# Kernel tuning notes

Measured on AMD Instinct MI355X. Metric: run time of the kernel, lower is better.

## Reference

```python
import jax, jax.numpy as jnp
import numpy as np

B, S, HID = 1, 2048, 4096
NH, NKV, HD = 32, 8, 128
N_REP = NH // NKV
EPS = 1e-5
ROPE_THETA = 500000.0


def setup_inputs() -> dict:
    key = jax.random.key(0)
    ks = jax.random.split(key, 16)
    s = 0.02
    return {
        "hidden_states": jax.random.normal(ks[0], (B, S, HID), jnp.float32),
        "Wq": jax.random.normal(ks[1], (NH * HD, HID), jnp.float32) * s,
        "bq": jnp.zeros((NH * HD,), jnp.float32),
        "Wk": jax.random.normal(ks[2], (NKV * HD, HID), jnp.float32) * s,
        "bk": jnp.zeros((NKV * HD,), jnp.float32),
        "Wv": jax.random.normal(ks[3], (NKV * HD, HID), jnp.float32) * s,
        "bv": jnp.zeros((NKV * HD,), jnp.float32),
        "Wo": jax.random.normal(ks[4], (HID, HID), jnp.float32) * s,
        "bo": jnp.zeros((HID,), jnp.float32),
        "qn_g": jnp.ones((HD,), jnp.float32),
        "qn_b": jnp.zeros((HD,), jnp.float32),
        "kn_g": jnp.ones((HD,), jnp.float32),
        "kn_b": jnp.zeros((HD,), jnp.float32),
    }


def _layernorm(x, g, b):
    mu = jnp.mean(x, axis=-1, keepdims=True)
    var = jnp.var(x, axis=-1, keepdims=True)
    return (x - mu) * jax.lax.rsqrt(var + EPS) * g + b


def _rope_tables(seq_len, dtype):
    inv_freq = 1.0 / ROPE_THETA ** (jnp.arange(0, HD, 2, dtype=jnp.float32) / HD)
    pos = jnp.arange(seq_len, dtype=jnp.float32)
    freqs = pos[:, None] * inv_freq[None, :]          # (S, HD/2)
    emb = jnp.concatenate([freqs, freqs], axis=-1)    # (S, HD)
    return jnp.cos(emb).astype(dtype), jnp.sin(emb).astype(dtype)


def _rotate_half(x):
    x1, x2 = x[..., : HD // 2], x[..., HD // 2 :]
    return jnp.concatenate([-x2, x1], axis=-1)


def reference(hidden_states, Wq, bq, Wk, bk, Wv, bv, Wo, bo, qn_g, qn_b, kn_g, kn_b):
    x = hidden_states
    q = (x @ Wq.T + bq).reshape(B, S, NH, HD)
    k = (x @ Wk.T + bk).reshape(B, S, NKV, HD)
    v = (x @ Wv.T + bv).reshape(B, S, NKV, HD)
    # QK-Norm (LayerNorm over head_dim)
    q = _layernorm(q, qn_g, qn_b).transpose(0, 2, 1, 3)  # (B, NH, S, HD)
    k = _layernorm(k, kn_g, kn_b).transpose(0, 2, 1, 3)  # (B, NKV, S, HD)
    v = v.transpose(0, 2, 1, 3)
    # RoPE
    cos, sin = _rope_tables(S, x.dtype)  # (S, HD) each, broadcast over B, heads
    q = q * cos + _rotate_half(q) * sin
    k = k * cos + _rotate_half(k) * sin
    # GQA: repeat KV heads
    k = jnp.repeat(k, N_REP, axis=1)  # (B, NH, S, HD)
    v = jnp.repeat(v, N_REP, axis=1)
    # Causal attention
    scores = jnp.einsum("bhqd,bhkd->bhqk", q, k) / jnp.sqrt(jnp.float32(HD)).astype(x.dtype)
    causal = jnp.tril(jnp.ones((S, S), bool))
    scores = jnp.where(causal, scores, jnp.finfo(scores.dtype).min)
    attn = jax.nn.softmax(scores, axis=-1)
    out = jnp.einsum("bhqk,bhkd->bhqd", attn, v)
    out = out.transpose(0, 2, 1, 3).reshape(B, S, HID)
    return out @ Wo.T + bo
```

## Files before the change

kernel.cpp:

```cpp
#include <hip/hip_runtime.h>

typedef __bf16 bf16;
typedef __bf16 bf16x8 __attribute__((ext_vector_type(8)));
typedef __bf16 bf16x4 __attribute__((ext_vector_type(4)));
typedef float f32x4 __attribute__((ext_vector_type(4)));

#define S_LEN 2048
#define HID 4096
#define NH 32
#define NKV 8
#define HD 128
#define QSTR 6144
#define SCALE 0.08838834764831845f
#define QSCL 0.1275164918918885f
#define M2C 16.33f

template <int V> struct IC { static constexpr int value = V; };

__device__ __forceinline__ bf16x8 load8(const bf16* p) { return *(const bf16x8*)p; }
__device__ __forceinline__ bf16x8 load8(const float* p) {
    float4 a = *(const float4*)p;
    float4 b = *(const float4*)(p + 4);
    bf16x8 r;
    r[0] = (bf16)a.x; r[1] = (bf16)a.y; r[2] = (bf16)a.z; r[3] = (bf16)a.w;
    r[4] = (bf16)b.x; r[5] = (bf16)b.y; r[6] = (bf16)b.z; r[7] = (bf16)b.w;
    return r;
}

__device__ __forceinline__ void load_lds16(const bf16* g, bf16* l) {
    __builtin_amdgcn_global_load_lds(
        (const __attribute__((address_space(1))) void*)g,
        (__attribute__((address_space(3))) void*)l, 16, 0, 0);
}

template <int C> __device__ __forceinline__ void vmwait_if() {
    if constexpr (C >= 0) asm volatile("s_waitcnt vmcnt(%0)" ::"n"(C) : "memory");
}

__device__ __forceinline__ void lgkm0() {
    asm volatile("s_waitcnt lgkmcnt(0)" ::: "memory");
    __builtin_amdgcn_sched_barrier(0);
}

__global__ __launch_bounds__(256) void cvt5(const float* __restrict__ x,
                                            const float* __restrict__ Wq,
                                            const float* __restrict__ Wk,
                                            const float* __restrict__ Wv,
                                            const float* __restrict__ Wo,
                                            bf16* __restrict__ xb,
                                            bf16* __restrict__ Wqkv,
                                            bf16* __restrict__ Wob) {
    int i = blockIdx.x * 256 + threadIdx.x;
    const float* src;
    bf16* dst;
    if (i < 1048576)      { src = x  + (size_t)i * 8;              dst = xb + (size_t)i * 8; }
    else if (i < 3145728) { size_t j = i - 1048576; src = Wq + j * 8; dst = Wqkv + j * 8; }
    else if (i < 3670016) { size_t j = i - 3145728; src = Wk + j * 8; dst = Wqkv + 16777216 + j * 8; }
    else if (i < 4194304) { size_t j = i - 3670016; src = Wv + j * 8; dst = Wqkv + 20971520 + j * 8; }
    else                  { size_t j = i - 4194304; src = Wo + j * 8; dst = Wob + j * 8; }
    *(bf16x8*)dst = load8(src);
}

template <int BMODE, typename TO>
__global__ __launch_bounds__(512, 2) void gemmQ(const bf16* __restrict__ A,
                                                const bf16* __restrict__ Bw,
                                                const float* __restrict__ b0,
                                                const float* __restrict__ b1,
                                                const float* __restrict__ b2,
                                                TO* __restrict__ out,
                                                int N, int K) {
    __shared__ __align__(16) bf16 AS[4 * 128 * 64];
    __shared__ __align__(16) bf16 BS[4 * 128 * 64];

    const int tid  = threadIdx.x;
    const int wave = tid >> 6;
    const int lane = tid & 63;
    const int quad = lane >> 4;
    const int l16  = lane & 15;
    const int wm   = wave >> 2;
    const int wn   = wave & 3;

    const int gx   = gridDim.x;
    const int nwg  = gx * gridDim.y;
    const int orig = blockIdx.y * gx + blockIdx.x;
    int wg = orig;
    if ((nwg & 7) == 0) wg = (orig & 7) * (nwg >> 3) + (orig >> 3);
    const int row0 = (wg / gx) * 256;
    const int col0 = (wg % gx) * 256;

    auto stageA = [&](int h, int bufv, int kt) {
#pragma unroll
        for (int j = 0; j < 2; ++j) {
            int c = j * 512 + tid;
            int r = c >> 3, pg = c & 7;
            int g = pg ^ (r & 7);
            int gr = (r >> 6) * 128 + h * 64 + (r & 63);
            load_lds16(&A[(size_t)(row0 + gr) * K + kt * 64 + g * 8],
                       &AS[(bufv * 2 + h) * 8192 + c * 8]);
        }
    };
    auto stageB = [&](int nh, int bufv, int kt) {
#pragma unroll
        for (int j = 0; j < 2; ++j) {
            int c = j * 512 + tid;
            int r = c >> 3, pg = c & 7;
            int g = pg ^ (r & 7);
            int gc = (r >> 5) * 64 + nh * 32 + (r & 31);
            load_lds16(&Bw[(size_t)(col0 + gc) * K + kt * 64 + g * 8],
                       &BS[(bufv * 2 + nh) * 8192 + c * 8]);
        }
    };

    f32x4 acc[8][4];
#pragma unroll
    for (int a = 0; a < 8; ++a)
#pragma unroll
        for (int b = 0; b < 4; ++b) { f32x4 z = {0.f, 0.f, 0.f, 0.f}; acc[a][b] = z; }

    bf16x8 afr[4][2];
    bf16x8 bfr[2][2][2];

    auto loadAh = [&](int h, int bufv) {
#pragma unroll
        for (int mi = 0; mi < 4; ++mi)
#pragma unroll
            for (int ks = 0; ks < 2; ++ks) {
                int r = wm * 64 + mi * 16 + l16;
                int gg = ks * 4 + quad;
                afr[mi][ks] = *(const bf16x8*)&AS[(bufv * 2 + h) * 8192 + r * 64 +
                                                  ((gg ^ (r & 7)) << 3)];
            }
    };
    auto loadBh = [&](auto cNQ, int bufv) {
        constexpr int NQ = decltype(cNQ)::value;
#pragma unroll
        for (int ni = 0; ni < 2; ++ni)
#pragma unroll
            for (int ks = 0; ks < 2; ++ks) {
                int r = wn * 32 + ni * 16 + l16;
                int gg = ks * 4 + quad;
                bfr[NQ][ni][ks] = *(const bf16x8*)&BS[(bufv * 2 + NQ) * 8192 + r * 64 +
                                                      ((gg ^ (r & 7)) << 3)];
            }
    };
    auto mmac = [&](auto cMQ, auto cNQ) {
        constexpr int MQ = decltype(cMQ)::value, NQ = decltype(cNQ)::value;
        __builtin_amdgcn_s_setprio(1);
#pragma unroll
        for (int mi = 0; mi < 4; ++mi)
#pragma unroll
            for (int ni = 0; ni < 2; ++ni)
#pragma unroll
                for (int ks = 0; ks < 2; ++ks)
                    acc[MQ * 4 + mi][NQ * 2 + ni] = __builtin_amdgcn_mfma_f32_16x16x32_bf16(
                        afr[mi][ks], bfr[NQ][ni][ks], acc[MQ * 4 + mi][NQ * 2 + ni], 0, 0, 0);
        __builtin_amdgcn_s_setprio(0);
    };

    auto run_iter = [&](int t0, auto cST, auto cV3, auto cV7) {
        constexpr bool ST = decltype(cST)::value != 0;
        stageA(1, 1, t0 + 1);
        loadAh(0, 0);
        loadBh(IC<0>{}, 0);
        __builtin_amdgcn_s_barrier();
        lgkm0();
        mmac(IC<0>{}, IC<0>{});
        __builtin_amdgcn_s_barrier();
        if constexpr (ST) stageA(0, 0, t0 + 2);
        loadBh(IC<1>{}, 0);
        __builtin_amdgcn_s_barrier();
        lgkm0();
        mmac(IC<0>{}, IC<1>{});
        __builtin_amdgcn_s_barrier();
        if constexpr (ST) stageB(0, 0, t0 + 2);
        loadAh(1, 0);
        __builtin_amdgcn_s_barrier();
        lgkm0();
        mmac(IC<1>{}, IC<0>{});
        __builtin_amdgcn_s_barrier();
        if constexpr (ST) stageB(1, 0, t0 + 2);
        __builtin_amdgcn_s_barrier();
        mmac(IC<1>{}, IC<1>{});
        vmwait_if<decltype(cV3)::value>();
        __builtin_amdgcn_s_barrier();
        if constexpr (ST) stageA(1, 0, t0 + 2);
        loadAh(0, 1);
        loadBh(IC<0>{}, 1);
        __builtin_amdgcn_s_barrier();
        lgkm0();
        mmac(IC<0>{}, IC<0>{});
        __builtin_amdgcn_s_barrier();
        if constexpr (ST) stageA(0, 1, t0 + 3);
        loadBh(IC<1>{}, 1);
        __builtin_amdgcn_s_barrier();
        lgkm0();
        mmac(IC<0>{}, IC<1>{});
        __builtin_amdgcn_s_barrier();
        if constexpr (ST) stageB(0, 1, t0 + 3);
        loadAh(1, 1);
        __builtin_amdgcn_s_barrier();
        lgkm0();
        mmac(IC<1>{}, IC<0>{});
        __builtin_amdgcn_s_barrier();
        if constexpr (ST) stageB(1, 1, t0 + 3);
        __builtin_amdgcn_s_barrier();
        mmac(IC<1>{}, IC<1>{});
        vmwait_if<decltype(cV7)::value>();
        __builtin_amdgcn_s_barrier();
    };

    stageA(0, 0, 0); stageB(0, 0, 0); stageB(1, 0, 0); stageA(1, 0, 0);
    stageA(0, 1, 1); stageB(0, 1, 1); stageB(1, 1, 1);
    vmwait_if<6>();
    __builtin_amdgcn_s_barrier();

    const int NT = K >> 6;
    for (int t0 = 0; t0 < NT - 2; t0 += 2)
        run_iter(t0, IC<1>{}, IC<6>{}, IC<6>{});
    run_iter(NT - 2, IC<0>{}, IC<0>{}, IC<-1>{});

#pragma unroll
    for (int mq = 0; mq < 2; ++mq)
#pragma unroll
        for (int nq = 0; nq < 2; ++nq)
#pragma unroll
            for (int ni = 0; ni < 2; ++ni) {
                int n = col0 + wn * 64 + nq * 32 + ni * 16 + l16;
                float bv;
                if (BMODE == 0) bv = b0[n];
                else bv = (n < 4096) ? b0[n] : ((n < 5120) ? b1[n - 4096] : b2[n - 5120]);
#pragma unroll
                for (int mi = 0; mi < 4; ++mi) {
                    int m = row0 + wm * 128 + mq * 64 + mi * 16 + quad * 4;
#pragma unroll
                    for (int reg = 0; reg < 4; ++reg)
                        out[(size_t)(m + reg) * N + n] =
                            (TO)(acc[mq * 4 + mi][nq * 2 + ni][reg] + bv);
                }
            }
}

template <int BM, int BN, int WM, int WN, int BMODE, typename TO>
__global__ __launch_bounds__(512, 2) void gemm8(const bf16* __restrict__ A,
                                                const bf16* __restrict__ Bw,
                                                const float* __restrict__ b0,
                                                const float* __restrict__ b1,
                                                const float* __restrict__ b2,
                                                TO* __restrict__ out,
                                                int N, int K) {
    constexpr int RW  = BM / WM;
    constexpr int CW  = BN / WN;
    constexpr int FM  = RW / 16;
    constexpr int FN  = CW / 16;
    constexpr int FMH = FM / 2;
    constexpr int FNH0 = (FN + 1) / 2, FNH1 = FN - FNH0;
    constexpr int SZ0 = FNH0 * 16, SZ1 = FNH1 * 16;
    constexpr int AROWS_H = BM / 2;
    constexpr int B0ROWS = WN * SZ0, B1ROWS = WN * SZ1;
    constexpr int LA  = AROWS_H / 64;
    constexpr int LB0 = B0ROWS / 64, LB1 = B1ROWS / 64;
    constexpr int V0  = 2 * LA + LB0;
    constexpr int V3  = 2 * LA + LB0 + LB1;
    constexpr int V3T = LA + LB1;

    __shared__ __align__(16) bf16 AS[2 * BM * 64];
    __shared__ __align__(16) bf16 BS[2 * BN * 64];

    const int tid  = threadIdx.x;
    const int wave = tid >> 6;
    const int lane = tid & 63;
    const int quad = lane >> 4;
    const int l16  = lane & 15;
    const int wm   = wave / WN;
    const int wn   = wave % WN;

    const int gx   = gridDim.x;
    const int nwg  = gx * gridDim.y;
    const int orig = blockIdx.y * gx + blockIdx.x;
    int wg = orig;
    if ((nwg & 7) == 0) wg = (orig & 7) * (nwg >> 3) + (orig >> 3);
    const int row0 = (wg / gx) * BM;
    const int col0 = (wg % gx) * BN;

    auto stageA = [&](int mh, int bufv, int kt) {
#pragma unroll
        for (int j = 0; j < LA; ++j) {
            int c = j * 512 + tid;
            int r = c >> 3, pg = c & 7;
            int g = pg ^ (r & 7);
            int gr = (r / (RW / 2)) * RW + mh * (RW / 2) + (r % (RW / 2));
            load_lds16(&A[(size_t)(row0 + gr) * K + kt * 64 + g * 8],
                       &AS[bufv * (BM * 64) + mh * (AROWS_H * 64) + c * 8]);
        }
    };
    auto stageB0 = [&](int bufv, int kt) {
#pragma unroll
        for (int j = 0; j < LB0; ++j) {
            int c = j * 512 + tid;
            int r = c >> 3, pg = c & 7;
            int g = pg ^ (r & 7);
            int gc = (r / SZ0) * CW + (r % SZ0);
            load_lds16(&Bw[(size_t)(col0 + gc) * K + kt * 64 + g * 8],
                       &BS[bufv * (BN * 64) + c * 8]);
        }
    };
    auto stageB1 = [&](int bufv, int kt) {
#pragma unroll
        for (int j = 0; j < LB1; ++j) {
            int c = j * 512 + tid;
            int r = c >> 3, pg = c & 7;
            int g = pg ^ (r & 7);
            int gc = (r / SZ1) * CW + SZ0 + (r % SZ1);
            load_lds16(&Bw[(size_t)(col0 + gc) * K + kt * 64 + g * 8],
                       &BS[bufv * (BN * 64) + B0ROWS * 64 + c * 8]);
        }
    };

    f32x4 acc[FM][FN];
#pragma unroll
    for (int mi = 0; mi < FM; ++mi)
#pragma unroll
        for (int ni = 0; ni < FN; ++ni) { f32x4 z = {0.f, 0.f, 0.f, 0.f}; acc[mi][ni] = z; }

    bf16x8 af[FMH][2];
    bf16x8 bfv[FN][2];

    auto loadA = [&](int mh, int bufv) {
#pragma unroll
        for (int mi = 0; mi < FMH; ++mi)
#pragma unroll
            for (int ks = 0; ks < 2; ++ks) {
                int r = wm * (RW / 2) + mi * 16 + l16;
                int g = ks * 4 + quad;
                af[mi][ks] = *(const bf16x8*)&AS[bufv * (BM * 64) + mh * (AROWS_H * 64) +
                                                 r * 64 + ((g ^ (r & 7)) << 3)];
            }
    };
    auto loadB = [&](auto cNH, int bufv) {
        constexpr int NHv = decltype(cNH)::value;
        constexpr int CNT = NHv ? FNH1 : FNH0;
        constexpr int SZ  = NHv ? SZ1 : SZ0;
#pragma unroll
        for (int nj = 0; nj < CNT; ++nj)
#pragma unroll
            for (int ks = 0; ks < 2; ++ks) {
                int r = wn * SZ + nj * 16 + l16;
                int g = ks * 4 + quad;
                bfv[NHv * FNH0 + nj][ks] =
                    *(const bf16x8*)&BS[bufv * (BN * 64) + NHv * (B0ROWS * 64) +
                                        r * 64 + ((g ^ (r & 7)) << 3)];
            }
    };
    auto mmac = [&](auto cMH, auto cNH) {
        constexpr int MH = decltype(cMH)::value, NHv = decltype(cNH)::value;
        constexpr int NB = NHv ? FNH0 : 0, NE = NHv ? FN : FNH0;
        __builtin_amdgcn_s_setprio(1);
#pragma unroll
        for (int mi = 0; mi < FMH; ++mi)
#pragma unroll
            for (int ni = NB; ni < NE; ++ni)
#pragma unroll
                for (int ks = 0; ks < 2; ++ks)
                    acc[MH * FMH + mi][ni] = __builtin_amdgcn_mfma_f32_16x16x32_bf16(
                        af[mi][ks], bfv[ni][ks], acc[MH * FMH + mi][ni], 0, 0, 0);
        __builtin_amdgcn_s_setprio(0);
    };

    auto run_tile = [&](int t, auto cSA1, auto cSB1, auto cSA0, auto cSB0,
                        auto cV0, auto cV3) {
        const int buf = t & 1, nbuf = buf ^ 1;
        loadA(0, buf);
        loadB(IC<0>{}, buf);
        if constexpr (decltype(cSA1)::value) stageA(1, nbuf, t + 1);
        __builtin_amdgcn_s_barrier();
        lgkm0();
        mmac(IC<0>{}, IC<0>{});
        vmwait_if<decltype(cV0)::value>();
        __builtin_amdgcn_s_barrier();
        loadB(IC<1>{}, buf);
        if constexpr (decltype(cSB1)::value) stageB1(nbuf, t + 1);
        __builtin_amdgcn_s_barrier();
        lgkm0();
        mmac(IC<0>{}, IC<1>{});
        __builtin_amdgcn_s_barrier();
        loadA(1, buf);
        if constexpr (decltype(cSA0)::value) stageA(0, buf, t + 2);
        __builtin_amdgcn_s_barrier();
        lgkm0();
        mmac(IC<1>{}, IC<0>{});
        __builtin_amdgcn_s_barrier();
        if constexpr (decltype(cSB0)::value) stageB0(buf, t + 2);
        __builtin_amdgcn_s_barrier();
        lgkm0();
        mmac(IC<1>{}, IC<1>{});
        vmwait_if<decltype(cV3)::value>();
        __builtin_amdgcn_s_barrier();
    };

    stageA(0, 0, 0); stageB0(0, 0);
    stageA(1, 0, 0); stageB1(0, 0);
    stageA(0, 1, 1); stageB0(1, 1);
    vmwait_if<V3>();
    __builtin_amdgcn_s_barrier();

    const int NT = K >> 6;
    for (int t = 0; t < NT - 2; ++t)
        run_tile(t, IC<1>{}, IC<1>{}, IC<1>{}, IC<1>{}, IC<V0>{}, IC<V3>{});
    run_tile(NT - 2, IC<1>{}, IC<1>{}, IC<0>{}, IC<0>{}, IC<V0>{}, IC<V3T>{});
    run_tile(NT - 1, IC<0>{}, IC<0>{}, IC<0>{}, IC<0>{}, IC<0>{}, IC<-1>{});

#pragma unroll
    for (int ni = 0; ni < FN; ++ni) {
        int n = col0 + wn * CW + ni * 16 + l16;
        float bv;
        if (BMODE == 0) bv = b0[n];
        else bv = (n < 4096) ? b0[n] : ((n < 5120) ? b1[n - 4096] : b2[n - 5120]);
#pragma unroll
        for (int mi = 0; mi < FM; ++mi) {
            int m = row0 + wm * RW + mi * 16 + quad * 4;
#pragma unroll
            for (int reg = 0; reg < 4; ++reg)
                out[(size_t)(m + reg) * N + n] = (TO)(acc[mi][ni][reg] + bv);
        }
    }
}

__global__ __launch_bounds__(256) void ln_rope(bf16* __restrict__ qkv,
                                               const float* __restrict__ qg, const float* __restrict__ qbt,
                                               const float* __restrict__ kg, const float* __restrict__ kbt) {
    int row  = blockIdx.x * 4 + (threadIdx.x >> 6);
    int lane = threadIdx.x & 63;

    bf16* ptr;
    const float *g, *bb;
    int s;
    float osc;
    if (row < S_LEN * NH) {
        s   = row >> 5;
        ptr = qkv + (size_t)s * QSTR + (row & 31) * HD;
        g   = qg; bb = qbt; osc = QSCL;
    } else {
        int r2 = row - S_LEN * NH;
        s   = r2 >> 3;
        ptr = qkv + (size_t)s * QSTR + 4096 + (r2 & 7) * HD;
        g   = kg; bb = kbt; osc = 1.f;
    }

    float x1 = (float)ptr[lane];
    float x2 = (float)ptr[lane + 64];
    float sum = x1 + x2;
    float sq  = x1 * x1 + x2 * x2;
#pragma unroll
    for (int m = 1; m < 64; m <<= 1) {
        sum += __shfl_xor(sum, m);
        sq  += __shfl_xor(sq, m);
    }
    float mu  = sum * (1.f / 128.f);
    float var = sq * (1.f / 128.f) - mu * mu;
    float rs  = rsqrtf(var + 1e-5f);
    float n1  = (x1 - mu) * rs * g[lane] + bb[lane];
    float n2  = (x2 - mu) * rs * g[lane + 64] + bb[lane + 64];

    float inv = exp2f(-0.2958057514f * (float)lane);
    float ang = (float)s * inv;
    float sn, cs;
    sincosf(ang, &sn, &cs);

    ptr[lane]      = (bf16)((n1 * cs - n2 * sn) * osc);
    ptr[lane + 64] = (bf16)((n2 * cs + n1 * sn) * osc);
}

__global__ __launch_bounds__(256) void transpose_v(const bf16* __restrict__ qkv,
                                                   bf16* __restrict__ vT) {
    __shared__ bf16 Ts[64 * 64];
    const int c0 = blockIdx.x * 64;
    const int s0 = blockIdx.y * 64;
    const int tid = threadIdx.x;

#pragma unroll
    for (int i = 0; i < 2; ++i) {
        int cc = i * 256 + tid;
        int r = cc >> 3, col8 = cc & 7;
        *(bf16x8*)&Ts[r * 64 + ((col8 ^ (r & 7)) << 3)] =
            *(const bf16x8*)&qkv[(size_t)(s0 + r) * QSTR + 5120 + c0 + (col8 << 3)];
    }
    __syncthreads();
#pragma unroll
    for (int i = 0; i < 2; ++i) {
        int oc = i * 256 + tid;
        int c = oc & 63, sb = oc >> 6;
        bf16x8 r8;
#pragma unroll
        for (int j = 0; j < 8; ++j) {
            int sg = sb * 8 + j;
            r8[j] = Ts[sg * 64 + ((((c >> 3) ^ (sg & 7)) << 3) + (c & 7))];
        }
        *(bf16x8*)&vT[(size_t)(c0 + c) * S_LEN + s0 + sb * 8] = r8;
    }
}

__global__ __launch_bounds__(512) void attn4(const bf16* __restrict__ qkv,
                                             const bf16* __restrict__ vT,
                                             bf16* __restrict__ abuf) {
    const int pairp = blockIdx.x;
    const int kvh   = blockIdx.y;
    const int tid   = threadIdx.x;
    const int wave  = tid >> 6;
    const int lane  = tid & 63;
    const int quad  = lane >> 4;
    const int l16   = lane & 15;
    const int spw   = wave >> 2;
    const int hw    = wave & 3;
    const int h     = kvh * 4 + hw;

    __shared__ __align__(16) bf16 smem[2 * 64 * 128 + 2 * 128 * 64 + 8 * 32 * 64];
    __shared__ float Ls[8][32];
    bf16* Ksb = smem;
    bf16* Vtb = smem + 2 * 64 * 128;
    bf16* Psb = smem + 2 * 64 * 128 + 2 * 128 * 64;

    bf16x8 onesf;
#pragma unroll
    for (int j = 0; j < 8; ++j) onesf[j] = (bf16)1.f;

    int4 pk[4], pv[4];

    for (int ph = 0; ph < 2; ++ph) {
        const int qt  = ph ? (63 - pairp) : pairp;
        const int r0  = qt * 32;
        const int nkt = qt / 2 + 1;
        const int nit = (nkt + 1) >> 1;

        bf16x8 qf[2][4];
#pragma unroll
        for (int mi = 0; mi < 2; ++mi)
#pragma unroll
            for (int ks = 0; ks < 4; ++ks)
                qf[mi][ks] = *(const bf16x8*)&qkv[(size_t)(r0 + mi * 16 + l16) * QSTR +
                                                  h * HD + ks * 32 + quad * 8];

        f32x4 o_acc[2][8];
#pragma unroll
        for (int mi = 0; mi < 2; ++mi)
#pragma unroll
            for (int ni = 0; ni < 8; ++ni) {
                f32x4 z = {0.f, 0.f, 0.f, 0.f};
                o_acc[mi][ni] = z;
            }
        f32x4 lacc[2];
#pragma unroll
        for (int mi = 0; mi < 2; ++mi) { f32x4 z = {0.f, 0.f, 0.f, 0.f}; lacc[mi] = z; }

        auto load_regs = [&](int kt0) {
#pragma unroll
            for (int i = 0; i < 4; ++i) {
                int cc = i * 512 + tid;
                int tile = cc >> 10, g = cc & 1023;
                int key = g >> 4, d8 = g & 15;
                pk[i] = *(const int4*)&qkv[(size_t)((kt0 + tile) * 64 + key) * QSTR + 4096 +
                                           kvh * HD + (d8 << 3)];
            }
#pragma unroll
            for (int i = 0; i < 4; ++i) {
                int cc = i * 512 + tid;
                int tile = cc >> 10, g = cc & 1023;
                int d = g >> 3, k8 = g & 7;
                pv[i] = *(const int4*)&vT[(size_t)(kvh * HD + d) * S_LEN +
                                          (kt0 + tile) * 64 + (k8 << 3)];
            }
        };

        load_regs(0);

        for (int it = 0; it < nit; ++it) {
#pragma unroll
            for (int i = 0; i < 4; ++i) {
                int cc = i * 512 + tid;
                int tile = cc >> 10, g = cc & 1023;
                int key = g >> 4, d8 = g & 15;
                *(int4*)&Ksb[tile * 8192 + key * 128 + ((d8 ^ (key & 7)) << 3)] = pk[i];
            }
#pragma unroll
            for (int i = 0; i < 4; ++i) {
                int cc = i * 512 + tid;
                int tile = cc >> 10, g = cc & 1023;
                int d = g >> 3, k8 = g & 7;
                *(int4*)&Vtb[tile * 8192 + d * 64 + ((k8 ^ (d & 7)) << 3)] = pv[i];
            }
            __syncthreads();

            if (it + 1 < nit) load_regs(2 * (it + 1));

            const int kt = 2 * it + spw;
            if (kt < nkt) {
                const bf16* Kw = Ksb + spw * 8192;
                const bf16* Vw = Vtb + spw * 8192;
                bf16* Pw = Psb + wave * 2048;

                f32x4 sacc[2][4];
#pragma unroll
                for (int mi = 0; mi < 2; ++mi)
#pragma unroll
                    for (int ni = 0; ni < 4; ++ni) {
                        f32x4 z = {0.f, 0.f, 0.f, 0.f};
                        sacc[mi][ni] = z;
                    }
#pragma unroll
                for (int ks = 0; ks < 4; ++ks)
#pragma unroll
                    for (int ni = 0; ni < 4; ++ni) {
                        bf16x8 kf = *(const bf16x8*)&Kw[(ni * 16 + l16) * 128 +
                                                        ((((ks << 2) + quad) ^ (l16 & 7)) << 3)];
                        sacc[0][ni] = __builtin_amdgcn_mfma_f32_16x16x32_bf16(qf[0][ks], kf, sacc[0][ni], 0, 0, 0);
                        sacc[1][ni] = __builtin_amdgcn_mfma_f32_16x16x32_bf16(qf[1][ks], kf, sacc[1][ni], 0, 0, 0);
                    }

#pragma unroll
                for (int mi = 0; mi < 2; ++mi)
#pragma unroll
                    for (int reg = 0; reg < 4; ++reg) {
                        int rloc = mi * 16 + quad * 4 + reg;
                        int qrow = r0 + rloc;
#pragma unroll
                        for (int ni = 0; ni < 4; ++ni) {
                            int key = kt * 64 + ni * 16 + l16;
                            float t = (key > qrow) ? -1e30f : (sacc[mi][ni][reg] - M2C);
                            float p = exp2f(t);
                            int blk = (ni * 2 + (l16 >> 3)) ^ (rloc & 7);
                            Pw[rloc * 64 + blk * 8 + (l16 & 7)] = (bf16)p;
                        }
                    }

#pragma unroll
                for (int ks2 = 0; ks2 < 2; ++ks2) {
                    bf16x8 pa[2];
#pragma unroll
                    for (int mi = 0; mi < 2; ++mi) {
                        int rloc = mi * 16 + l16;
                        pa[mi] = *(const bf16x8*)&Pw[rloc * 64 +
                                                     ((((ks2 << 2) + quad) ^ (rloc & 7)) << 3)];
                    }
#pragma unroll
                    for (int ni = 0; ni < 8; ++ni) {
                        int d = ni * 16 + l16;
                        bf16x8 vf = *(const bf16x8*)&Vw[d * 64 + ((((ks2 << 2) + quad) ^ (d & 7)) << 3)];
                        o_acc[0][ni] = __builtin_amdgcn_mfma_f32_16x16x32_bf16(pa[0], vf, o_acc[0][ni], 0, 0, 0);
                        o_acc[1][ni] = __builtin_amdgcn_mfma_f32_16x16x32_bf16(pa[1], vf, o_acc[1][ni], 0, 0, 0);
                    }
                    lacc[0] = __builtin_amdgcn_mfma_f32_16x16x32_bf16(pa[0], onesf, lacc[0], 0, 0, 0);
                    lacc[1] = __builtin_amdgcn_mfma_f32_16x16x32_bf16(pa[1], onesf, lacc[1], 0, 0, 0);
                }
            }
            __syncthreads();
        }

        float* M = (float*)smem;
        if (spw == 1) {
            float* Mw = M + hw * 4096;
#pragma unroll
            for (int mi = 0; mi < 2; ++mi)
#pragma unroll
                for (int ni = 0; ni < 8; ++ni)
#pragma unroll
                    for (int j = 0; j < 4; ++j)
                        Mw[((mi * 8 + ni) * 4 + j) * 64 + lane] = o_acc[mi][ni][j];
            if (l16 == 0)
#pragma unroll
                for (int mi = 0; mi < 2; ++mi)
#pragma unroll
                    for (int reg = 0; reg < 4; ++reg)
                        Ls[wave][mi * 16 + quad * 4 + reg] = lacc[mi][reg];
        }
        __syncthreads();
        if (spw == 0) {
            float* Mw = M + hw * 4096;
#pragma unroll
            for (int mi = 0; mi < 2; ++mi) {
                float linv[4];
#pragma unroll
                for (int reg = 0; reg < 4; ++reg)
                    linv[reg] = 1.f / fmaxf(lacc[mi][reg] +
                                            Ls[wave + 4][mi * 16 + quad * 4 + reg], 1e-30f);
#pragma unroll
                for (int ni = 0; ni < 8; ++ni)
#pragma unroll
                    for (int reg = 0; reg < 4; ++reg) {
                        float v = o_acc[mi][ni][reg] + Mw[((mi * 8 + ni) * 4 + reg) * 64 + lane];
                        int s = r0 + mi * 16 + quad * 4 + reg;
                        abuf[(size_t)s * HID + h * HD + ni * 16 + l16] = (bf16)(v * linv[reg]);
                    }
            }
        }
        __syncthreads();
    }
}

template <typename TA, typename TO>
__global__ __launch_bounds__(256) void gemm_bt(const TA* __restrict__ A,
                                               const float* __restrict__ W,
                                               const float* __restrict__ bias,
                                               TO* __restrict__ out,
                                               int N, int K) {
    __shared__ __align__(16) bf16 As[128 * 64];
    __shared__ __align__(16) bf16 Bs[128 * 64];
    const int tid = threadIdx.x, wave = tid >> 6, lane = tid & 63;
    const int quad = lane >> 4, l16 = lane & 15, wm = wave >> 1, wn = wave & 1;
    const int row0 = blockIdx.y * 128, col0 = blockIdx.x * 128;
    f32x4 acc[4][4];
#pragma unroll
    for (int mi = 0; mi < 4; ++mi)
#pragma unroll
        for (int ni = 0; ni < 4; ++ni) { f32x4 z = {0.f,0.f,0.f,0.f}; acc[mi][ni] = z; }
    for (int k0 = 0; k0 < K; k0 += 64) {
#pragma unroll
        for (int i = 0; i < 4; ++i) {
            int c = i * 256 + tid, r = c >> 3, col8 = (c & 7) << 3;
            *(bf16x8*)&As[r * 64 + col8] = load8(&A[(size_t)(row0 + r) * K + k0 + col8]);
            *(bf16x8*)&Bs[r * 64 + col8] = load8(&W[(size_t)(col0 + r) * K + k0 + col8]);
        }
        __syncthreads();
#pragma unroll
        for (int ks = 0; ks < 2; ++ks) {
            bf16x8 af[4], bfr[4];
#pragma unroll
            for (int mi = 0; mi < 4; ++mi)
                af[mi] = *(const bf16x8*)&As[(wm * 64 + mi * 16 + l16) * 64 + ks * 32 + quad * 8];
#pragma unroll
            for (int ni = 0; ni < 4; ++ni)
                bfr[ni] = *(const bf16x8*)&Bs[(wn * 64 + ni * 16 + l16) * 64 + ks * 32 + quad * 8];
#pragma unroll
            for (int mi = 0; mi < 4; ++mi)
#pragma unroll
                for (int ni = 0; ni < 4; ++ni)
                    acc[mi][ni] = __builtin_amdgcn_mfma_f32_16x16x32_bf16(af[mi], bfr[ni], acc[mi][ni], 0, 0, 0);
        }
        __syncthreads();
    }
#pragma unroll
    for (int ni = 0; ni < 4; ++ni) {
        int n = col0 + wn * 64 + ni * 16 + l16;
        float bv = bias[n];
#pragma unroll
        for (int mi = 0; mi < 4; ++mi) {
            int m = row0 + wm * 64 + mi * 16 + quad * 4;
#pragma unroll
            for (int reg = 0; reg < 4; ++reg)
                out[(size_t)(m + reg) * N + n] = (TO)(acc[mi][ni][reg] + bv);
        }
    }
}

__global__ __launch_bounds__(256) void ln_rope_f(bf16* __restrict__ qb, bf16* __restrict__ kb,
                                                 const float* __restrict__ qg, const float* __restrict__ qbt,
                                                 const float* __restrict__ kg, const float* __restrict__ kbt) {
    int row = blockIdx.x * 4 + (threadIdx.x >> 6);
    int lane = threadIdx.x & 63;
    bf16* ptr; const float *g, *bb; int s;
    if (row < S_LEN * NH) { s = row >> 5; ptr = qb + (size_t)s * (NH * HD) + (row & 31) * HD; g = qg; bb = qbt; }
    else { int r2 = row - S_LEN * NH; s = r2 >> 3; ptr = kb + (size_t)s * (NKV * HD) + (r2 & 7) * HD; g = kg; bb = kbt; }
    float x1 = (float)ptr[lane], x2 = (float)ptr[lane + 64];
    float sum = x1 + x2, sq = x1 * x1 + x2 * x2;
#pragma unroll
    for (int m = 1; m < 64; m <<= 1) { sum += __shfl_xor(sum, m); sq += __shfl_xor(sq, m); }
    float mu = sum * (1.f / 128.f), var = sq * (1.f / 128.f) - mu * mu;
    float rs = rsqrtf(var + 1e-5f);
    float n1 = (x1 - mu) * rs * g[lane] + bb[lane];
    float n2 = (x2 - mu) * rs * g[lane + 64] + bb[lane + 64];
    float inv = powf(500000.f, -(float)lane * (1.f / 64.f));
    float ang = (float)s * inv, sn, cs;
    sincosf(ang, &sn, &cs);
    ptr[lane] = (bf16)(n1 * cs - n2 * sn);
    ptr[lane + 64] = (bf16)(n2 * cs + n1 * sn);
}

__global__ __launch_bounds__(256) void attn_old(const bf16* __restrict__ qbuf,
                                                const bf16* __restrict__ kbuf,
                                                const bf16* __restrict__ vbuf,
                                                bf16* __restrict__ obuf) {
    const int qi = blockIdx.x, hh = blockIdx.y, kvh = hh >> 2;
    __shared__ __align__(16) bf16 Qs[64 * 128];
    __shared__ __align__(16) bf16 Ks2[64 * 128];
    __shared__ __align__(16) bf16 Vt2[128 * 80];
    __shared__ __align__(16) float Ss[64 * 64];
    __shared__ __align__(16) bf16 Ps2[64 * 64];
    __shared__ float mS[64], lS[64], aS[64];
    const int tid = threadIdx.x, wave = tid >> 6, lane = tid & 63;
    const int quad = lane >> 4, l16 = lane & 15;
#pragma unroll
    for (int i = 0; i < 4; ++i) {
        int c = i * 256 + tid, r = c >> 4, col8 = (c & 15) << 3;
        *(int4*)&Qs[r * 128 + col8] = *(const int4*)&qbuf[(size_t)(qi * 64 + r) * HID + hh * HD + col8];
    }
    if (tid < 64) { mS[tid] = -1e30f; lS[tid] = 0.f; }
    f32x4 o_acc[8];
#pragma unroll
    for (int i = 0; i < 8; ++i) { f32x4 z = {0.f,0.f,0.f,0.f}; o_acc[i] = z; }
    __syncthreads();
    for (int kt = 0; kt <= qi; ++kt) {
#pragma unroll
        for (int i = 0; i < 4; ++i) {
            int c = i * 256 + tid, r = c >> 4, col8 = (c & 15) << 3;
            const size_t gofs = (size_t)(kt * 64 + r) * (NKV * HD) + kvh * HD + col8;
            *(int4*)&Ks2[r * 128 + col8] = *(const int4*)&kbuf[gofs];
            bf16x8 vv = *(const bf16x8*)&vbuf[gofs];
#pragma unroll
            for (int e = 0; e < 8; ++e) Vt2[(col8 + e) * 80 + r] = vv[e];
        }
        __syncthreads();
        f32x4 sacc[4];
#pragma unroll
        for (int ni = 0; ni < 4; ++ni) { f32x4 z = {0.f,0.f,0.f,0.f}; sacc[ni] = z; }
#pragma unroll
        for (int ks = 0; ks < 4; ++ks) {
            bf16x8 a = *(const bf16x8*)&Qs[(wave * 16 + l16) * 128 + ks * 32 + quad * 8];
#pragma unroll
            for (int ni = 0; ni < 4; ++ni) {
                bf16x8 b = *(const bf16x8*)&Ks2[(ni * 16 + l16) * 128 + ks * 32 + quad * 8];
                sacc[ni] = __builtin_amdgcn_mfma_f32_16x16x32_bf16(a, b, sacc[ni], 0, 0, 0);
            }
        }
#pragma unroll
        for (int ni = 0; ni < 4; ++ni)
#pragma unroll
            for (int reg = 0; reg < 4; ++reg) {
                int r = wave * 16 + quad * 4 + reg, cc = ni * 16 + l16;
                float sv = sacc[ni][reg] * SCALE;
                if (kt * 64 + cc > qi * 64 + r) sv = -1e30f;
                Ss[r * 64 + cc] = sv;
            }
        __syncthreads();
        {
            int r = tid >> 2, j = tid & 3;
            float vals[16], mloc = -1e30f;
#pragma unroll
            for (int c = 0; c < 16; ++c) { vals[c] = Ss[r * 64 + j * 16 + c]; mloc = fmaxf(mloc, vals[c]); }
            mloc = fmaxf(mloc, __shfl_xor(mloc, 1));
            mloc = fmaxf(mloc, __shfl_xor(mloc, 2));
            float mold = mS[r], mnew = fmaxf(mold, mloc), ssum = 0.f;
#pragma unroll
            for (int c = 0; c < 16; ++c) {
                float p = __expf(vals[c] - mnew);
                ssum += p;
                Ps2[r * 64 + j * 16 + c] = (bf16)p;
            }
            ssum += __shfl_xor(ssum, 1);
            ssum += __shfl_xor(ssum, 2);
            if (j == 0) { float alpha = __expf(mold - mnew); mS[r] = mnew; lS[r] = lS[r] * alpha + ssum; aS[r] = alpha; }
        }
        __syncthreads();
        {
            float al2[4];
#pragma unroll
            for (int reg = 0; reg < 4; ++reg) al2[reg] = aS[wave * 16 + quad * 4 + reg];
#pragma unroll
            for (int ni = 0; ni < 8; ++ni)
#pragma unroll
                for (int reg = 0; reg < 4; ++reg) o_acc[ni][reg] *= al2[reg];
#pragma unroll
            for (int ks = 0; ks < 2; ++ks) {
                bf16x8 a = *(const bf16x8*)&Ps2[(wave * 16 + l16) * 64 + ks * 32 + quad * 8];
#pragma unroll
                for (int ni = 0; ni < 8; ++ni) {
                    bf16x8 b = *(const bf16x8*)&Vt2[(ni * 16 + l16) * 80 + ks * 32 + quad * 8];
                    o_acc[ni] = __builtin_amdgcn_mfma_f32_16x16x32_bf16(a, b, o_acc[ni], 0, 0, 0);
                }
            }
        }
        __syncthreads();
    }
    {
        float linv[4];
#pragma unroll
        for (int reg = 0; reg < 4; ++reg) linv[reg] = 1.f / fmaxf(lS[wave * 16 + quad * 4 + reg], 1e-20f);
#pragma unroll
        for (int ni = 0; ni < 8; ++ni)
#pragma unroll
            for (int reg = 0; reg < 4; ++reg) {
                int r = wave * 16 + quad * 4 + reg;
                obuf[(size_t)(qi * 64 + r) * HID + hh * HD + ni * 16 + l16] = (bf16)(o_acc[ni][reg] * linv[reg]);
            }
    }
}

extern "C" void kernel_launch(void* const* d_in, const int* in_sizes, int n_in,
                              void* d_out, int out_size, void* d_ws, size_t ws_size,
                              hipStream_t stream) {
    const float* x   = (const float*)d_in[0];
    const float* Wq  = (const float*)d_in[1];
    const float* bq  = (const float*)d_in[2];
    const float* Wk  = (const float*)d_in[3];
    const float* bk  = (const float*)d_in[4];
    const float* Wv  = (const float*)d_in[5];
    const float* bv  = (const float*)d_in[6];
    const float* Wo  = (const float*)d_in[7];
    const float* bo  = (const float*)d_in[8];
    const float* qg  = (const float*)d_in[9];
    const float* qbt = (const float*)d_in[10];
    const float* kg  = (const float*)d_in[11];
    const float* kbt = (const float*)d_in[12];
    float* out = (float*)d_out;

    const size_t NEED = 130547712;
    if (ws_size >= NEED) {
        char* p = (char*)d_ws;
        bf16*  xb   = (bf16*)p;
        bf16*  Wqkv = (bf16*)(p + 16777216);
        bf16*  abuf = (bf16*)p;
        bf16*  Wob  = (bf16*)(p + 67108864);
        bf16*  qkv  = (bf16*)(p + 100663296);
        bf16*  vT   = (bf16*)(p + 125829120);

        cvt5<<<24576, 256, 0, stream>>>(x, Wq, Wk, Wv, Wo, xb, Wqkv, Wob);

        gemmQ<1, bf16><<<dim3(24, 8), 512, 0, stream>>>(
            xb, Wqkv, bq, bk, bv, qkv, QSTR, 4096);

        ln_rope<<<dim3((S_LEN * (NH + NKV)) / 4), 256, 0, stream>>>(qkv, qg, qbt, kg, kbt);

        transpose_v<<<dim3(16, 32), 256, 0, stream>>>(qkv, vT);

        attn4<<<dim3(32, 8), 512, 0, stream>>>(qkv, vT, abuf);

        gemm8<256, 128, 4, 2, 0, float><<<dim3(32, 8), 512, 0, stream>>>(
            abuf, Wob, bo, bo, bo, out, 4096, 4096);
    } else {
        char* ws = (char*)d_ws;
        bf16* qbuf = (bf16*)(ws);
        bf16* kbuf = (bf16*)(ws + (16u << 20));
        bf16* vbuf = (bf16*)(ws + (20u << 20));
        bf16* abuf = (bf16*)(ws + (24u << 20));
        gemm_bt<float, bf16><<<dim3(32, 16), 256, 0, stream>>>(x, Wq, bq, qbuf, 4096, 4096);
        gemm_bt<float, bf16><<<dim3(8, 16), 256, 0, stream>>>(x, Wk, bk, kbuf, 1024, 4096);
        gemm_bt<float, bf16><<<dim3(8, 16), 256, 0, stream>>>(x, Wv, bv, vbuf, 1024, 4096);
        ln_rope_f<<<dim3((S_LEN * (NH + NKV)) / 4), 256, 0, stream>>>(qbuf, kbuf, qg, qbt, kg, kbt);
        attn_old<<<dim3(32, 32), 256, 0, stream>>>(qbuf, kbuf, vbuf, abuf);
        gemm_bt<bf16, float><<<dim3(32, 16), 256, 0, stream>>>(abuf, Wo, bo, out, 4096, 4096);
    }
}
```

Measured before the change: 559.1 us.

## Restructure attention: one query tile per block, 4 waves, double-buffered KV

Replaces the 512-thread attention kernel, which split key tiles across two wave groups, processed two query tiles per block and merged partial results through shared memory. The new kernel gives each 256-thread block a single query tile and walks all key tiles itself with a double-buffered K/V pipeline, so the cross-group merge disappears. It doubles the grid, pairs short and long tiles through the blockIdx-to-tile mapping for load balance, asks for two blocks per CU, and wraps the MFMA sections in s_setprio. The trade is half as many waves per query tile working in parallel, so each block runs a longer serial loop over keys.

```diff
diff --git a/kernel.cpp b/kernel.cpp
--- a/kernel.cpp
+++ b/kernel.cpp
@@ -499,199 +499,171 @@
     }
 }
 
-__global__ __launch_bounds__(512) void attn4(const bf16* __restrict__ qkv,
-                                             const bf16* __restrict__ vT,
-                                             bf16* __restrict__ abuf) {
-    const int pairp = blockIdx.x;
-    const int kvh   = blockIdx.y;
-    const int tid   = threadIdx.x;
-    const int wave  = tid >> 6;
-    const int lane  = tid & 63;
-    const int quad  = lane >> 4;
-    const int l16   = lane & 15;
-    const int spw   = wave >> 2;
-    const int hw    = wave & 3;
-    const int h     = kvh * 4 + hw;
-
-    __shared__ __align__(16) bf16 smem[2 * 64 * 128 + 2 * 128 * 64 + 8 * 32 * 64];
-    __shared__ float Ls[8][32];
+__global__ __launch_bounds__(256, 2) void attn5(const bf16* __restrict__ qkv,
+                                                const bf16* __restrict__ vT,
+                                                bf16* __restrict__ abuf) {
+    const int lin = blockIdx.y * 64 + blockIdx.x;
+    int qt, kvh;
+    if (lin < 256) { qt = lin & 63;        kvh = lin >> 6; }
+    else           { qt = 63 - (lin & 63); kvh = 4 + ((lin - 256) >> 6); }
+
+    const int tid  = threadIdx.x;
+    const int wave = tid >> 6;
+    const int lane = tid & 63;
+    const int quad = lane >> 4;
+    const int l16  = lane & 15;
+    const int h    = kvh * 4 + wave;
+    const int r0   = qt * 32;
+    const int nkt  = qt / 2 + 1;
+
+    __shared__ __align__(16) bf16 smem[2 * 8192 + 2 * 8192 + 4 * 2048];
     bf16* Ksb = smem;
-    bf16* Vtb = smem + 2 * 64 * 128;
-    bf16* Psb = smem + 2 * 64 * 128 + 2 * 128 * 64;
+    bf16* Vtb = smem + 2 * 8192;
+    bf16* Psb = smem + 4 * 8192;
 
     bf16x8 onesf;
 #pragma unroll
     for (int j = 0; j < 8; ++j) onesf[j] = (bf16)1.f;
 
+    bf16x8 qf[2][4];
+#pragma unroll
+    for (int mi = 0; mi < 2; ++mi)
+#pragma unroll
+        for (int ks = 0; ks < 4; ++ks)
+            qf[mi][ks] = *(const bf16x8*)&qkv[(size_t)(r0 + mi * 16 + l16) * QSTR +
+                                              h * HD + ks * 32 + quad * 8];
+
+    f32x4 o_acc[2][8];
+#pragma unroll
+    for (int mi = 0; mi < 2; ++mi)
+#pragma unroll
+        for (int ni = 0; ni < 8; ++ni) {
+            f32x4 z = {0.f, 0.f, 0.f, 0.f};
+            o_acc[mi][ni] = z;
+        }
+    f32x4 lacc[2];
+#pragma unroll
+    for (int mi = 0; mi < 2; ++mi) { f32x4 z = {0.f, 0.f, 0.f, 0.f}; lacc[mi] = z; }
+
     int4 pk[4], pv[4];
-
-    for (int ph = 0; ph < 2; ++ph) {
-        const int qt  = ph ? (63 - pairp) : pairp;
-        const int r0  = qt * 32;
-        const int nkt = qt / 2 + 1;
-        const int nit = (nkt + 1) >> 1;
-
-        bf16x8 qf[2][4];
+    auto load_regs = [&](int kt) {
+#pragma unroll
+        for (int i = 0; i < 4; ++i) {
+            int cc = i * 256 + tid;
+            int key = cc >> 4, d8 = cc & 15;
+            pk[i] = *(const int4*)&qkv[(size_t)(kt * 64 + key) * QSTR + 4096 +
+                                       kvh * HD + (d8 << 3)];
+        }
+#pragma unroll
+        for (int i = 0; i < 4; ++i) {
+            int cc = i * 256 + tid;
+            int d = cc >> 3, k8 = cc & 7;
+            pv[i] = *(const int4*)&vT[(size_t)(kvh * HD + d) * S_LEN + kt * 64 + (k8 << 3)];
+        }
+    };
+    auto drain = [&](int b) {
+#pragma unroll
+        for (int i = 0; i < 4; ++i) {
+            int cc = i * 256 + tid;
+            int key = cc >> 4, d8 = cc & 15;
+            *(int4*)&Ksb[b * 8192 + key * 128 + ((d8 ^ (key & 7)) << 3)] = pk[i];
+        }
+#pragma unroll
+        for (int i = 0; i < 4; ++i) {
+            int cc = i * 256 + tid;
+            int d = cc >> 3, k8 = cc & 7;
+            *(int4*)&Vtb[b * 8192 + d * 64 + ((k8 ^ (d & 7)) << 3)] = pv[i];
+        }
+    };
+
+    load_regs(0);
+    drain(0);
+    __syncthreads();
+
+    for (int kt = 0; kt < nkt; ++kt) {
+        const int b = kt & 1;
+        if (kt + 1 < nkt) load_regs(kt + 1);
+
+        const bf16* Kw = Ksb + b * 8192;
+        const bf16* Vw = Vtb + b * 8192;
+        bf16* Pw = Psb + wave * 2048;
+
+        f32x4 sacc[2][4];
 #pragma unroll
         for (int mi = 0; mi < 2; ++mi)
 #pragma unroll
-            for (int ks = 0; ks < 4; ++ks)
-                qf[mi][ks] = *(const bf16x8*)&qkv[(size_t)(r0 + mi * 16 + l16) * QSTR +
-                                                  h * HD + ks * 32 + quad * 8];
-
-        f32x4 o_acc[2][8];
+            for (int ni = 0; ni < 4; ++ni) {
+                f32x4 z = {0.f, 0.f, 0.f, 0.f};
+                sacc[mi][ni] = z;
+            }
+        __builtin_amdgcn_s_setprio(1);
+#pragma unroll
+        for (int ks = 0; ks < 4; ++ks)
+#pragma unroll
+            for (int ni = 0; ni < 4; ++ni) {
+                bf16x8 kf = *(const bf16x8*)&Kw[(ni * 16 + l16) * 128 +
+                                                ((((ks << 2) + quad) ^ (l16 & 7)) << 3)];
+                sacc[0][ni] = __builtin_amdgcn_mfma_f32_16x16x32_bf16(qf[0][ks], kf, sacc[0][ni], 0, 0, 0);
+                sacc[1][ni] = __builtin_amdgcn_mfma_f32_16x16x32_bf16(qf[1][ks], kf, sacc[1][ni], 0, 0, 0);
+            }
+        __builtin_amdgcn_s_setprio(0);
+
 #pragma unroll
         for (int mi = 0; mi < 2; ++mi)
 #pragma unroll
+            for (int reg = 0; reg < 4; ++reg) {
+                int rloc = mi * 16 + quad * 4 + reg;
+                int qrow = r0 + rloc;
+#pragma unroll
+                for (int ni = 0; ni < 4; ++ni) {
+                    int key = kt * 64 + ni * 16 + l16;
+                    float t = (key > qrow) ? -1e30f : (sacc[mi][ni][reg] - M2C);
+                    float p = exp2f(t);
+                    int blk = (ni * 2 + (l16 >> 3)) ^ (rloc & 7);
+                    Pw[rloc * 64 + blk * 8 + (l16 & 7)] = (bf16)p;
+                }
+            }
+
+        __builtin_amdgcn_s_setprio(1);
+#pragma unroll
+        for (int ks2 = 0; ks2 < 2; ++ks2) {
+            bf16x8 pa[2];
+#pragma unroll
+            for (int mi = 0; mi < 2; ++mi) {
+                int rloc = mi * 16 + l16;
+                pa[mi] = *(const bf16x8*)&Pw[rloc * 64 +
+                                             ((((ks2 << 2) + quad) ^ (rloc & 7)) << 3)];
+            }
+#pragma unroll
             for (int ni = 0; ni < 8; ++ni) {
-                f32x4 z = {0.f, 0.f, 0.f, 0.f};
-                o_acc[mi][ni] = z;
-            }
-        f32x4 lacc[2];
-#pragma unroll
-        for (int mi = 0; mi < 2; ++mi) { f32x4 z = {0.f, 0.f, 0.f, 0.f}; lacc[mi] = z; }
-
-        auto load_regs = [&](int kt0) {
-#pragma unroll
-            for (int i = 0; i < 4; ++i) {
-                int cc = i * 512 + tid;
-                int tile = cc >> 10, g = cc & 1023;
-                int key = g >> 4, d8 = g & 15;
-                pk[i] = *(const int4*)&qkv[(size_t)((kt0 + tile) * 64 + key) * QSTR + 4096 +
-                                           kvh * HD + (d8 << 3)];
-            }
-#pragma unroll
-            for (int i = 0; i < 4; ++i) {
-                int cc = i * 512 + tid;
-                int tile = cc >> 10, g = cc & 1023;
-                int d = g >> 3, k8 = g & 7;
-                pv[i] = *(const int4*)&vT[(size_t)(kvh * HD + d) * S_LEN +
-                                          (kt0 + tile) * 64 + (k8 << 3)];
-            }
-        };
-
-        load_regs(0);
-
-        for (int it = 0; it < nit; ++it) {
-#pragma unroll
-            for (int i = 0; i < 4; ++i) {
-                int cc = i * 512 + tid;
-                int tile = cc >> 10, g = cc & 1023;
-                int key = g >> 4, d8 = g & 15;
-                *(int4*)&Ksb[tile * 8192 + key * 128 + ((d8 ^ (key & 7)) << 3)] = pk[i];
-            }
-#pragma unroll
-            for (int i = 0; i < 4; ++i) {
-                int cc = i * 512 + tid;
-                int tile = cc >> 10, g = cc & 1023;
-                int d = g >> 3, k8 = g & 7;
-                *(int4*)&Vtb[tile * 8192 + d * 64 + ((k8 ^ (d & 7)) << 3)] = pv[i];
-            }
-            __syncthreads();
-
-            if (it + 1 < nit) load_regs(2 * (it + 1));
-
-            const int kt = 2 * it + spw;
-            if (kt < nkt) {
-                const bf16* Kw = Ksb + spw * 8192;
-                const bf16* Vw = Vtb + spw * 8192;
-                bf16* Pw = Psb + wave * 2048;
-
-                f32x4 sacc[2][4];
-#pragma unroll
-                for (int mi = 0; mi < 2; ++mi)
-#pragma unroll
-                    for (int ni = 0; ni < 4; ++ni) {
-                        f32x4 z = {0.f, 0.f, 0.f, 0.f};
-                        sacc[mi][ni] = z;
-                    }
-#pragma unroll
-                for (int ks = 0; ks < 4; ++ks)
-#pragma unroll
-                    for (int ni = 0; ni < 4; ++ni) {
-                        bf16x8 kf = *(const bf16x8*)&Kw[(ni * 16 + l16) * 128 +
-                                                        ((((ks << 2) + quad) ^ (l16 & 7)) << 3)];
-                        sacc[0][ni] = __builtin_amdgcn_mfma_f32_16x16x32_bf16(qf[0][ks], kf, sacc[0][ni], 0, 0, 0);
-                        sacc[1][ni] = __builtin_amdgcn_mfma_f32_16x16x32_bf16(qf[1][ks], kf, sacc[1][ni], 0, 0, 0);
-                    }
-
-#pragma unroll
-                for (int mi = 0; mi < 2; ++mi)
-#pragma unroll
-                    for (int reg = 0; reg < 4; ++reg) {
-                        int rloc = mi * 16 + quad * 4 + reg;
-                        int qrow = r0 + rloc;
-#pragma unroll
-                        for (int ni = 0; ni < 4; ++ni) {
-                            int key = kt * 64 + ni * 16 + l16;
-                            float t = (key > qrow) ? -1e30f : (sacc[mi][ni][reg] - M2C);
-                            float p = exp2f(t);
-                            int blk = (ni * 2 + (l16 >> 3)) ^ (rloc & 7);
-                            Pw[rloc * 64 + blk * 8 + (l16 & 7)] = (bf16)p;
-                        }
-                    }
-
-#pragma unroll
-                for (int ks2 = 0; ks2 < 2; ++ks2) {
-                    bf16x8 pa[2];
-#pragma unroll
-                    for (int mi = 0; mi < 2; ++mi) {
-                        int rloc = mi * 16 + l16;
-                        pa[mi] = *(const bf16x8*)&Pw[rloc * 64 +
-                                                     ((((ks2 << 2) + quad) ^ (rloc & 7)) << 3)];
-                    }
-#pragma unroll
-                    for (int ni = 0; ni < 8; ++ni) {
-                        int d = ni * 16 + l16;
-                        bf16x8 vf = *(const bf16x8*)&Vw[d * 64 + ((((ks2 << 2) + quad) ^ (d & 7)) << 3)];
-                        o_acc[0][ni] = __builtin_amdgcn_mfma_f32_16x16x32_bf16(pa[0], vf, o_acc[0][ni], 0, 0, 0);
-                        o_acc[1][ni] = __builtin_amdgcn_mfma_f32_16x16x32_bf16(pa[1], vf, o_acc[1][ni], 0, 0, 0);
-                    }
-                    lacc[0] = __builtin_amdgcn_mfma_f32_16x16x32_bf16(pa[0], onesf, lacc[0], 0, 0, 0);
-                    lacc[1] = __builtin_amdgcn_mfma_f32_16x16x32_bf16(pa[1], onesf, lacc[1], 0, 0, 0);
-                }
-            }
-            __syncthreads();
-        }
-
-        float* M = (float*)smem;
-        if (spw == 1) {
-            float* Mw = M + hw * 4096;
-#pragma unroll
-            for (int mi = 0; mi < 2; ++mi)
-#pragma unroll
-                for (int ni = 0; ni < 8; ++ni)
-#pragma unroll
-                    for (int j = 0; j < 4; ++j)
-                        Mw[((mi * 8 + ni) * 4 + j) * 64 + lane] = o_acc[mi][ni][j];
-            if (l16 == 0)
-#pragma unroll
-                for (int mi = 0; mi < 2; ++mi)
-#pragma unroll
-                    for (int reg = 0; reg < 4; ++reg)
-                        Ls[wave][mi * 16 + quad * 4 + reg] = lacc[mi][reg];
-        }
+                int d = ni * 16 + l16;
+                bf16x8 vf = *(const bf16x8*)&Vw[d * 64 + ((((ks2 << 2) + quad) ^ (d & 7)) << 3)];
+                o_acc[0][ni] = __builtin_amdgcn_mfma_f32_16x16x32_bf16(pa[0], vf, o_acc[0][ni], 0, 0, 0);
+                o_acc[1][ni] = __builtin_amdgcn_mfma_f32_16x16x32_bf16(pa[1], vf, o_acc[1][ni], 0, 0, 0);
+            }
+            lacc[0] = __builtin_amdgcn_mfma_f32_16x16x32_bf16(pa[0], onesf, lacc[0], 0, 0, 0);
+            lacc[1] = __builtin_amdgcn_mfma_f32_16x16x32_bf16(pa[1], onesf, lacc[1], 0, 0, 0);
+        }
+        __builtin_amdgcn_s_setprio(0);
+
+        if (kt + 1 < nkt) drain(b ^ 1);
         __syncthreads();
-        if (spw == 0) {
-            float* Mw = M + hw * 4096;
-#pragma unroll
-            for (int mi = 0; mi < 2; ++mi) {
-                float linv[4];
-#pragma unroll
-                for (int reg = 0; reg < 4; ++reg)
-                    linv[reg] = 1.f / fmaxf(lacc[mi][reg] +
-                                            Ls[wave + 4][mi * 16 + quad * 4 + reg], 1e-30f);
-#pragma unroll
-                for (int ni = 0; ni < 8; ++ni)
-#pragma unroll
-                    for (int reg = 0; reg < 4; ++reg) {
-                        float v = o_acc[mi][ni][reg] + Mw[((mi * 8 + ni) * 4 + reg) * 64 + lane];
-                        int s = r0 + mi * 16 + quad * 4 + reg;
-                        abuf[(size_t)s * HID + h * HD + ni * 16 + l16] = (bf16)(v * linv[reg]);
-                    }
-            }
-        }
-        __syncthreads();
+    }
+
+#pragma unroll
+    for (int mi = 0; mi < 2; ++mi) {
+        float linv[4];
+#pragma unroll
+        for (int reg = 0; reg < 4; ++reg)
+            linv[reg] = 1.f / fmaxf(lacc[mi][reg], 1e-30f);
+#pragma unroll
+        for (int reg = 0; reg < 4; ++reg) {
+            int s = r0 + mi * 16 + quad * 4 + reg;
+#pragma unroll
+            for (int ni = 0; ni < 8; ++ni)
+                abuf[(size_t)s * HID + h * HD + ni * 16 + l16] =
+                    (bf16)(o_acc[mi][ni][reg] * linv[reg]);
+        }
     }
 }
 
@@ -919,7 +891,7 @@
 
         transpose_v<<<dim3(16, 32), 256, 0, stream>>>(qkv, vT);
 
-        attn4<<<dim3(32, 8), 512, 0, stream>>>(qkv, vT, abuf);
+        attn5<<<dim3(64, 8), 256, 0, stream>>>(qkv, vT, abuf);
 
         gemm8<256, 128, 4, 2, 0, float><<<dim3(32, 8), 512, 0, stream>>>(
             abuf, Wob, bo, bo, bo, out, 4096, 4096);
```

After: 571.3 us. 2.2% more time.
